# Kernel tuning notes

Hardware: AMD Instinct MI355X
Metric: run time of the kernel (lower is better)

Reference implementation:

```python
import jax, jax.numpy as jnp
import numpy as np

T, B = 256, 64
VOCAB, EMBED, HIDDEN, LAYERS, TAGS = 50000, 512, 512, 2, 9
H = HIDDEN // 2  # per-direction hidden size


def setup_inputs() -> dict:
    key = jax.random.key(0)
    ks = jax.random.split(key, 11)
    s = 0.05
    embed_table = jax.random.normal(ks[1], (VOCAB, EMBED), dtype=jnp.float32) * s
    embed_table = embed_table.at[0].set(0.0)  # padding_idx=0 row is zero
    return {
        "x": jax.random.randint(ks[0], (T, B), 1, VOCAB),  # ids >=1 -> full lengths
        "embed_table": embed_table,
        "w_ih": jax.random.normal(ks[2], (LAYERS, 2, 4 * H, HIDDEN), dtype=jnp.float32) * s,
        "w_hh": jax.random.normal(ks[3], (LAYERS, 2, 4 * H, H), dtype=jnp.float32) * s,
        "b_ih": jax.random.normal(ks[4], (LAYERS, 2, 4 * H), dtype=jnp.float32) * s,
        "b_hh": jax.random.normal(ks[5], (LAYERS, 2, 4 * H), dtype=jnp.float32) * s,
        "out_w": jax.random.normal(ks[6], (TAGS, HIDDEN), dtype=jnp.float32) * s,
        "out_b": jax.random.normal(ks[7], (TAGS,), dtype=jnp.float32) * s,
        "start_trans": jax.random.normal(ks[8], (TAGS,), dtype=jnp.float32) * s,
        "end_trans": jax.random.normal(ks[9], (TAGS,), dtype=jnp.float32) * s,
        "trans": jax.random.normal(ks[10], (TAGS, TAGS), dtype=jnp.float32) * s,
    }


def _lstm_dir(xs, Wih, Whh, b, reverse):
    """One LSTM direction over time-major xs [T,B,D]; PyTorch gate order i,f,g,o."""
    bsz = xs.shape[1]
    h0 = jnp.zeros((bsz, H), xs.dtype)
    c0 = jnp.zeros((bsz, H), xs.dtype)

    def step(carry, xt):
        h, c = carry
        g = xt @ Wih.T + h @ Whh.T + b
        i, f, gg, o = jnp.split(g, 4, axis=-1)
        c = jax.nn.sigmoid(f) * c + jax.nn.sigmoid(i) * jnp.tanh(gg)
        h = jax.nn.sigmoid(o) * jnp.tanh(c)
        return (h, c), h

    _, hs = jax.lax.scan(step, (h0, c0), xs, reverse=reverse)
    return hs  # [T,B,H], aligned to input time order


def _emissions(x, embed_table, w_ih, w_hh, b_ih, b_hh, out_w, out_b):
    seq = embed_table[x]  # [T,B,EMBED]
    for l in range(LAYERS):
        fwd = _lstm_dir(seq, w_ih[l, 0], w_hh[l, 0], b_ih[l, 0] + b_hh[l, 0], False)
        bwd = _lstm_dir(seq, w_ih[l, 1], w_hh[l, 1], b_ih[l, 1] + b_hh[l, 1], True)
        seq = jnp.concatenate([fwd, bwd], axis=-1)  # [T,B,HIDDEN]
    return seq @ out_w.T + out_b  # [T,B,TAGS]


def reference(x, embed_table, w_ih, w_hh, b_ih, b_hh, out_w, out_b,
              start_trans, end_trans, trans):
    em = _emissions(x, embed_table, w_ih, w_hh, b_ih, b_hh, out_w, out_b)

    # Viterbi decode (all sequences full-length since ids >= 1)
    score0 = start_trans[None, :] + em[0]  # [B,TAGS]

    def vstep(score, em_t):
        tot = score[:, :, None] + trans[None, :, :]  # [B,prev,cur]
        best_prev = jnp.argmax(tot, axis=1)          # [B,cur]
        return jnp.max(tot, axis=1) + em_t, best_prev

    score, history = jax.lax.scan(vstep, score0, em[1:])  # history: [T-1,B,TAGS]
    score = score + end_trans[None, :]
    best_last = jnp.argmax(score, axis=-1)   # [B]
    best_score = jnp.max(score, axis=-1)     # [B]

    def btstep(tag, idx_t):
        prev = jnp.take_along_axis(idx_t, tag[:, None], axis=1)[:, 0]
        return prev, prev

    _, prevs = jax.lax.scan(btstep, best_last, history, reverse=True)  # [T-1,B]
    tags = jnp.concatenate([prevs, best_last[None, :]], axis=0)        # [T,B]
    return tags.T, best_score  # ([B,T] best paths, [B] path scores)
```

## Files before the change

### kernel.cpp

```cpp
#include <hip/hip_runtime.h>
#include <math.h>

#define TAGS 9

static __device__ __forceinline__ float sigmoidf_(float x) {
  return 1.0f / (1.0f + expf(-x));
}

__global__ void k_transpose_whh(const float* __restrict__ whh, float* __restrict__ whhT) {
  __shared__ float tile[64][65];
  int bid = blockIdx.x;
  int ld = bid >> 6;
  int rt = (bid >> 2) & 15;
  int kt = bid & 3;
  const float* in = whh + (size_t)ld * 1024 * 256;
  float* out = whhT + (size_t)ld * 256 * 1024;
  int tid = threadIdx.x;
  int lr = tid >> 6;
  int lc = tid & 63;
#pragma unroll
  for (int i = 0; i < 16; i++) {
    int r = rt * 64 + i * 4 + lr;
    tile[lc][i * 4 + lr] = in[(size_t)r * 256 + kt * 64 + lc];
  }
  __syncthreads();
#pragma unroll
  for (int i = 0; i < 16; i++) {
    int k = kt * 64 + i * 4 + lr;
    out[(size_t)k * 1024 + rt * 64 + lc] = tile[i * 4 + lr][lc];
  }
}

__global__ void k_gather(const int* __restrict__ x, const float* __restrict__ table,
                         float* __restrict__ seq) {
  int tid = blockIdx.x * 256 + threadIdx.x;
  int row = tid >> 7;
  int e4 = tid & 127;
  int idx = x[row];
  const float4* src = (const float4*)(table + (size_t)idx * 512);
  float4* dst = (float4*)(seq + (size_t)row * 512);
  dst[e4] = src[e4];
}

__global__ __launch_bounds__(256, 2)
void k_gemm_nt(const float* __restrict__ A, const float* __restrict__ W,
               const float* __restrict__ bias1, const float* __restrict__ bias2,
               float* __restrict__ C, int M, int N, int K) {
  __shared__ float As[16][132];
  __shared__ float Ws[16][132];
  int tid = threadIdx.x;
  int tx = tid & 15, ty = tid >> 4;
  int n0 = blockIdx.x * 128, m0 = blockIdx.y * 128;
  int lr = tid >> 2;
  int lk = (tid & 3) * 4;
  float acc[8][8];
#pragma unroll
  for (int i = 0; i < 8; i++)
#pragma unroll
    for (int j = 0; j < 8; j++) acc[i][j] = 0.f;
  const float* Ab = A + (size_t)m0 * K;
  const float* Wb = W + (size_t)n0 * K;
  for (int k0 = 0; k0 < K; k0 += 16) {
    float4 a0 = *(const float4*)&Ab[(size_t)lr * K + k0 + lk];
    float4 a1 = *(const float4*)&Ab[(size_t)(lr + 64) * K + k0 + lk];
    float4 w0 = *(const float4*)&Wb[(size_t)lr * K + k0 + lk];
    float4 w1 = *(const float4*)&Wb[(size_t)(lr + 64) * K + k0 + lk];
    __syncthreads();
    As[lk + 0][lr] = a0.x; As[lk + 1][lr] = a0.y; As[lk + 2][lr] = a0.z; As[lk + 3][lr] = a0.w;
    As[lk + 0][lr + 64] = a1.x; As[lk + 1][lr + 64] = a1.y; As[lk + 2][lr + 64] = a1.z; As[lk + 3][lr + 64] = a1.w;
    Ws[lk + 0][lr] = w0.x; Ws[lk + 1][lr] = w0.y; Ws[lk + 2][lr] = w0.z; Ws[lk + 3][lr] = w0.w;
    Ws[lk + 0][lr + 64] = w1.x; Ws[lk + 1][lr + 64] = w1.y; Ws[lk + 2][lr + 64] = w1.z; Ws[lk + 3][lr + 64] = w1.w;
    __syncthreads();
#pragma unroll
    for (int kk = 0; kk < 16; kk++) {
      float4 av0 = *(const float4*)&As[kk][ty * 4];
      float4 av1 = *(const float4*)&As[kk][ty * 4 + 64];
      float4 wv0 = *(const float4*)&Ws[kk][tx * 4];
      float4 wv1 = *(const float4*)&Ws[kk][tx * 4 + 64];
      float am[8] = {av0.x, av0.y, av0.z, av0.w, av1.x, av1.y, av1.z, av1.w};
      float wn[8] = {wv0.x, wv0.y, wv0.z, wv0.w, wv1.x, wv1.y, wv1.z, wv1.w};
#pragma unroll
      for (int i = 0; i < 8; i++)
#pragma unroll
        for (int j = 0; j < 8; j++) acc[i][j] += am[i] * wn[j];
    }
  }
  float bsum[8];
#pragma unroll
  for (int j = 0; j < 8; j++) {
    int n = n0 + ((j < 4) ? (tx * 4 + j) : (64 + tx * 4 + (j - 4)));
    bsum[j] = bias1[n] + bias2[n];
  }
#pragma unroll
  for (int i = 0; i < 8; i++) {
    int m = m0 + ((i < 4) ? (ty * 4 + i) : (64 + ty * 4 + (i - 4)));
    float4 o0 = {acc[i][0] + bsum[0], acc[i][1] + bsum[1], acc[i][2] + bsum[2], acc[i][3] + bsum[3]};
    float4 o1 = {acc[i][4] + bsum[4], acc[i][5] + bsum[5], acc[i][6] + bsum[6], acc[i][7] + bsum[7]};
    *(float4*)&C[(size_t)m * N + n0 + tx * 4] = o0;
    *(float4*)&C[(size_t)m * N + n0 + 64 + tx * 4] = o1;
  }
}

#define FMA4(ACC, WV, S) { ACC.x += WV.x * (S); ACC.y += WV.y * (S); ACC.z += WV.z * (S); ACC.w += WV.w * (S); }
__global__ __launch_bounds__(512, 1)
void k_lstm(const float* __restrict__ gates_in,
            const float* __restrict__ whhT2,
            float* __restrict__ seq_out) {
  int wg = blockIdx.x;
  int dir = wg & 1;
  int b0 = (wg >> 1) * 2;
  const float* wT = whhT2 + (size_t)dir * 256 * 1024;
  int tid = threadIdx.x;
  int kh = tid >> 8;
  int j4 = (tid & 255) * 4;
  int bs = kh, u = tid & 255;
  __shared__ float h_lds[2][256];
  __shared__ float part[2][2][1024];
  h_lds[kh][u] = 0.f;
  float c = 0.f;
  __syncthreads();
  const int khbase = kh * 128;
  const float* wbase = wT + (size_t)khbase * 1024 + j4;
  for (int tt = 0; tt < 256; tt++) {
    int t = dir ? (255 - tt) : tt;
    float4 acc0, acc1;
    if (kh == 0) {
      const float* gi = gates_in + (size_t)(t * 64 + b0) * 2048 + dir * 1024 + j4;
      acc0 = *(const float4*)gi;
      acc1 = *(const float4*)(gi + 2048);
    } else {
      acc0 = float4{0.f, 0.f, 0.f, 0.f};
      acc1 = float4{0.f, 0.f, 0.f, 0.f};
    }
#pragma unroll 4
    for (int k = 0; k < 128; k += 4) {
      float4 ha = *(const float4*)&h_lds[0][khbase + k];
      float4 hb = *(const float4*)&h_lds[1][khbase + k];
      const float* w = wbase + (size_t)k * 1024;
      float4 w0 = *(const float4*)(w);
      float4 w1 = *(const float4*)(w + 1024);
      float4 w2 = *(const float4*)(w + 2048);
      float4 w3 = *(const float4*)(w + 3072);
      FMA4(acc0, w0, ha.x) FMA4(acc0, w1, ha.y) FMA4(acc0, w2, ha.z) FMA4(acc0, w3, ha.w)
      FMA4(acc1, w0, hb.x) FMA4(acc1, w1, hb.y) FMA4(acc1, w2, hb.z) FMA4(acc1, w3, hb.w)
    }
    *(float4*)&part[kh][0][j4] = acc0;
    *(float4*)&part[kh][1][j4] = acc1;
    __syncthreads();
    float gi_ = part[0][bs][u]       + part[1][bs][u];
    float gf  = part[0][bs][256 + u] + part[1][bs][256 + u];
    float gg  = part[0][bs][512 + u] + part[1][bs][512 + u];
    float go  = part[0][bs][768 + u] + part[1][bs][768 + u];
    c = sigmoidf_(gf) * c + sigmoidf_(gi_) * tanhf(gg);
    float h = sigmoidf_(go) * tanhf(c);
    h_lds[bs][u] = h;
    seq_out[(size_t)(t * 64 + b0 + bs) * 512 + dir * 256 + u] = h;
    __syncthreads();
  }
}

__global__ void k_emis(const float* __restrict__ seq, const float* __restrict__ out_w,
                       const float* __restrict__ out_b, float* __restrict__ em) {
  __shared__ float ow[TAGS * 512];
  int tid = threadIdx.x;
  for (int i = tid; i < TAGS * 512; i += 256) ow[i] = out_w[i];
  __syncthreads();
  int lane = tid & 63;
  int row = blockIdx.x * 4 + (tid >> 6);
  const float* s = seq + (size_t)row * 512;
  float p[TAGS];
#pragma unroll
  for (int t = 0; t < TAGS; t++) p[t] = 0.f;
#pragma unroll
  for (int kk = 0; kk < 8; kk++) {
    float sv = s[lane + kk * 64];
#pragma unroll
    for (int t = 0; t < TAGS; t++) p[t] += sv * ow[t * 512 + lane + kk * 64];
  }
#pragma unroll
  for (int t = 0; t < TAGS; t++) {
    float v = p[t];
#pragma unroll
    for (int off = 32; off > 0; off >>= 1) v += __shfl_down(v, off, 64);
    if (lane == 0) em[(size_t)row * TAGS + t] = v + out_b[t];
  }
}

__global__ void k_viterbi(const float* __restrict__ em, const float* __restrict__ start_t,
                          const float* __restrict__ end_t, const float* __restrict__ trans,
                          float* __restrict__ out) {
  int b = blockIdx.x;
  int lane = threadIdx.x;
  __shared__ unsigned char hist[255 * TAGS];
  float tin[TAGS];
#pragma unroll
  for (int p = 0; p < TAGS; p++) tin[p] = (lane < TAGS) ? trans[p * TAGS + lane] : 0.f;
  float score = -1e30f;
  if (lane < TAGS) score = start_t[lane] + em[(size_t)b * TAGS + lane];
  for (int t = 1; t < 256; t++) {
    float best = -1e30f; int bp = 0;
#pragma unroll
    for (int p = 0; p < TAGS; p++) {
      float v = __shfl(score, p, 64) + tin[p];
      if (v > best) { best = v; bp = p; }
    }
    if (lane < TAGS) {
      score = best + em[(size_t)(t * 64 + b) * TAGS + lane];
      hist[(t - 1) * TAGS + lane] = (unsigned char)bp;
    }
  }
  float fin = (lane < TAGS) ? (score + end_t[lane]) : -1e30f;
  float bsc = -1e30f; int bl = 0;
#pragma unroll
  for (int p = 0; p < TAGS; p++) {
    float v = __shfl(fin, p, 64);
    if (v > bsc) { bsc = v; bl = p; }
  }
  __syncthreads();
  if (lane == 0) {
    out[(size_t)16384 + b] = bsc;
    int tag = bl;
    out[(size_t)b * 256 + 255] = (float)tag;
    for (int t = 254; t >= 0; t--) {
      tag = hist[t * TAGS + tag];
      out[(size_t)b * 256 + t] = (float)tag;
    }
  }
}

extern "C" void kernel_launch(void* const* d_in, const int* in_sizes, int n_in,
                              void* d_out, int out_size, void* d_ws, size_t ws_size,
                              hipStream_t stream) {
  const int*   x       = (const int*)d_in[0];
  const float* table   = (const float*)d_in[1];
  const float* w_ih    = (const float*)d_in[2];
  const float* w_hh    = (const float*)d_in[3];
  const float* b_ih    = (const float*)d_in[4];
  const float* b_hh    = (const float*)d_in[5];
  const float* out_w   = (const float*)d_in[6];
  const float* out_b   = (const float*)d_in[7];
  const float* start_t = (const float*)d_in[8];
  const float* end_t   = (const float*)d_in[9];
  const float* trans   = (const float*)d_in[10];
  float* out = (float*)d_out;
  float* ws = (float*)d_ws;

  float* whhT  = ws;
  float* seq0  = whhT + 1048576;
  float* seq1  = seq0 + 8388608;
  float* gates = seq1 + 8388608;
  float* em    = gates + 33554432;

  k_transpose_whh<<<256, 256, 0, stream>>>(w_hh, whhT);
  k_gather<<<8192, 256, 0, stream>>>(x, table, seq0);

  dim3 gg(16, 128);
  k_gemm_nt<<<gg, 256, 0, stream>>>(seq0, w_ih, b_ih, b_hh, gates, 16384, 2048, 512);
  k_lstm<<<64, 512, 0, stream>>>(gates, whhT, seq1);
  k_gemm_nt<<<gg, 256, 0, stream>>>(seq1, w_ih + 1048576, b_ih + 2048, b_hh + 2048, gates, 16384, 2048, 512);
  k_lstm<<<64, 512, 0, stream>>>(gates, whhT + 524288, seq0);
  k_emis<<<4096, 256, 0, stream>>>(seq0, out_w, out_b, em);
  k_viterbi<<<64, 64, 0, stream>>>(em, start_t, end_t, trans, out);
}
```

Baseline: 5.347 ms.

## Split LSTM recurrence across 256 workgroups with grid-wide barrier per timestep

The LSTM recurrence moves from 64 workgroups (each owning two batch rows and reading the full recurrent weight matrix from global memory every step) to 256 workgroups, each owning two hidden units for all 64 batch rows. Each workgroup keeps its small weight slice in LDS, exchanges h through a double-buffered global buffer, and synchronises every timestep with an atomic-counter grid barrier. The input-projection GEMM is transposed so it writes gates in a time/unit/batch layout matched to the new recurrence, and the separate weight-transpose kernel is dropped. This spreads the serial recurrence over more compute units and removes the repeated weight streaming. In exchange it adds 255 grid-wide barriers per layer, global round-trips of h, and relies on all 256 workgroups being co-resident.

```diff
diff --git a/kernel.cpp b/kernel.cpp
--- a/kernel.cpp
+++ b/kernel.cpp
@@ -2,33 +2,10 @@
 #include <math.h>
 
 #define TAGS 9
+#define NWG 256
 
 static __device__ __forceinline__ float sigmoidf_(float x) {
   return 1.0f / (1.0f + expf(-x));
-}
-
-__global__ void k_transpose_whh(const float* __restrict__ whh, float* __restrict__ whhT) {
-  __shared__ float tile[64][65];
-  int bid = blockIdx.x;
-  int ld = bid >> 6;
-  int rt = (bid >> 2) & 15;
-  int kt = bid & 3;
-  const float* in = whh + (size_t)ld * 1024 * 256;
-  float* out = whhT + (size_t)ld * 256 * 1024;
-  int tid = threadIdx.x;
-  int lr = tid >> 6;
-  int lc = tid & 63;
-#pragma unroll
-  for (int i = 0; i < 16; i++) {
-    int r = rt * 64 + i * 4 + lr;
-    tile[lc][i * 4 + lr] = in[(size_t)r * 256 + kt * 64 + lc];
-  }
-  __syncthreads();
-#pragma unroll
-  for (int i = 0; i < 16; i++) {
-    int k = kt * 64 + i * 4 + lr;
-    out[(size_t)k * 1024 + rt * 64 + lc] = tile[i * 4 + lr][lc];
-  }
 }
 
 __global__ void k_gather(const int* __restrict__ x, const float* __restrict__ table,
@@ -43,11 +20,11 @@
 }
 
 __global__ __launch_bounds__(256, 2)
-void k_gemm_nt(const float* __restrict__ A, const float* __restrict__ W,
-               const float* __restrict__ bias1, const float* __restrict__ bias2,
-               float* __restrict__ C, int M, int N, int K) {
+void k_gemm_gates(const float* __restrict__ A, const float* __restrict__ B,
+                  const float* __restrict__ bias1, const float* __restrict__ bias2,
+                  float* __restrict__ gatesT) {
   __shared__ float As[16][132];
-  __shared__ float Ws[16][132];
+  __shared__ float Bs[16][132];
   int tid = threadIdx.x;
   int tx = tid & 15, ty = tid >> 4;
   int n0 = blockIdx.x * 128, m0 = blockIdx.y * 128;
@@ -58,104 +35,151 @@
   for (int i = 0; i < 8; i++)
 #pragma unroll
     for (int j = 0; j < 8; j++) acc[i][j] = 0.f;
-  const float* Ab = A + (size_t)m0 * K;
-  const float* Wb = W + (size_t)n0 * K;
-  for (int k0 = 0; k0 < K; k0 += 16) {
-    float4 a0 = *(const float4*)&Ab[(size_t)lr * K + k0 + lk];
-    float4 a1 = *(const float4*)&Ab[(size_t)(lr + 64) * K + k0 + lk];
-    float4 w0 = *(const float4*)&Wb[(size_t)lr * K + k0 + lk];
-    float4 w1 = *(const float4*)&Wb[(size_t)(lr + 64) * K + k0 + lk];
+  const float* Ab = A + (size_t)m0 * 512;
+  const float* Bb = B + (size_t)n0 * 512;
+  for (int k0 = 0; k0 < 512; k0 += 16) {
+    float4 a0 = *(const float4*)&Ab[(size_t)lr * 512 + k0 + lk];
+    float4 a1 = *(const float4*)&Ab[(size_t)(lr + 64) * 512 + k0 + lk];
+    float4 w0 = *(const float4*)&Bb[(size_t)lr * 512 + k0 + lk];
+    float4 w1 = *(const float4*)&Bb[(size_t)(lr + 64) * 512 + k0 + lk];
     __syncthreads();
     As[lk + 0][lr] = a0.x; As[lk + 1][lr] = a0.y; As[lk + 2][lr] = a0.z; As[lk + 3][lr] = a0.w;
     As[lk + 0][lr + 64] = a1.x; As[lk + 1][lr + 64] = a1.y; As[lk + 2][lr + 64] = a1.z; As[lk + 3][lr + 64] = a1.w;
-    Ws[lk + 0][lr] = w0.x; Ws[lk + 1][lr] = w0.y; Ws[lk + 2][lr] = w0.z; Ws[lk + 3][lr] = w0.w;
-    Ws[lk + 0][lr + 64] = w1.x; Ws[lk + 1][lr + 64] = w1.y; Ws[lk + 2][lr + 64] = w1.z; Ws[lk + 3][lr + 64] = w1.w;
+    Bs[lk + 0][lr] = w0.x; Bs[lk + 1][lr] = w0.y; Bs[lk + 2][lr] = w0.z; Bs[lk + 3][lr] = w0.w;
+    Bs[lk + 0][lr + 64] = w1.x; Bs[lk + 1][lr + 64] = w1.y; Bs[lk + 2][lr + 64] = w1.z; Bs[lk + 3][lr + 64] = w1.w;
     __syncthreads();
 #pragma unroll
     for (int kk = 0; kk < 16; kk++) {
       float4 av0 = *(const float4*)&As[kk][ty * 4];
       float4 av1 = *(const float4*)&As[kk][ty * 4 + 64];
-      float4 wv0 = *(const float4*)&Ws[kk][tx * 4];
-      float4 wv1 = *(const float4*)&Ws[kk][tx * 4 + 64];
+      float4 bv0 = *(const float4*)&Bs[kk][tx * 4];
+      float4 bv1 = *(const float4*)&Bs[kk][tx * 4 + 64];
       float am[8] = {av0.x, av0.y, av0.z, av0.w, av1.x, av1.y, av1.z, av1.w};
-      float wn[8] = {wv0.x, wv0.y, wv0.z, wv0.w, wv1.x, wv1.y, wv1.z, wv1.w};
+      float bn[8] = {bv0.x, bv0.y, bv0.z, bv0.w, bv1.x, bv1.y, bv1.z, bv1.w};
 #pragma unroll
       for (int i = 0; i < 8; i++)
 #pragma unroll
-        for (int j = 0; j < 8; j++) acc[i][j] += am[i] * wn[j];
-    }
-  }
-  float bsum[8];
-#pragma unroll
-  for (int j = 0; j < 8; j++) {
-    int n = n0 + ((j < 4) ? (tx * 4 + j) : (64 + tx * 4 + (j - 4)));
-    bsum[j] = bias1[n] + bias2[n];
-  }
+        for (int j = 0; j < 8; j++) acc[i][j] += am[i] * bn[j];
+    }
+  }
+  int t0 = n0 >> 6;
 #pragma unroll
   for (int i = 0; i < 8; i++) {
     int m = m0 + ((i < 4) ? (ty * 4 + i) : (64 + ty * 4 + (i - 4)));
-    float4 o0 = {acc[i][0] + bsum[0], acc[i][1] + bsum[1], acc[i][2] + bsum[2], acc[i][3] + bsum[3]};
-    float4 o1 = {acc[i][4] + bsum[4], acc[i][5] + bsum[5], acc[i][6] + bsum[6], acc[i][7] + bsum[7]};
-    *(float4*)&C[(size_t)m * N + n0 + tx * 4] = o0;
-    *(float4*)&C[(size_t)m * N + n0 + 64 + tx * 4] = o1;
-  }
-}
-
-#define FMA4(ACC, WV, S) { ACC.x += WV.x * (S); ACC.y += WV.y * (S); ACC.z += WV.z * (S); ACC.w += WV.w * (S); }
-__global__ __launch_bounds__(512, 1)
-void k_lstm(const float* __restrict__ gates_in,
-            const float* __restrict__ whhT2,
-            float* __restrict__ seq_out) {
-  int wg = blockIdx.x;
-  int dir = wg & 1;
-  int b0 = (wg >> 1) * 2;
-  const float* wT = whhT2 + (size_t)dir * 256 * 1024;
-  int tid = threadIdx.x;
-  int kh = tid >> 8;
-  int j4 = (tid & 255) * 4;
-  int bs = kh, u = tid & 255;
-  __shared__ float h_lds[2][256];
-  __shared__ float part[2][2][1024];
-  h_lds[kh][u] = 0.f;
+    float bs = bias1[m] + bias2[m];
+    float4 o0 = {acc[i][0] + bs, acc[i][1] + bs, acc[i][2] + bs, acc[i][3] + bs};
+    float4 o1 = {acc[i][4] + bs, acc[i][5] + bs, acc[i][6] + bs, acc[i][7] + bs};
+    *(float4*)&gatesT[((size_t)t0 * 2048 + m) * 64 + tx * 4] = o0;
+    *(float4*)&gatesT[((size_t)(t0 + 1) * 2048 + m) * 64 + tx * 4] = o1;
+  }
+}
+
+__global__ __launch_bounds__(512)
+void k_lstm_rec(const float* __restrict__ gatesT,
+                const float* __restrict__ whh,
+                float* __restrict__ seq_out,
+                float* __restrict__ hbuf,
+                int* __restrict__ gbar,
+                int gen_base) {
+  __shared__ float h_s[256 * 64];
+  __shared__ float w_s[8][256];
+  __shared__ float g_p[64 * 64];
+  int wg = blockIdx.x, tid = threadIdx.x;
+  int d = wg & 1, ug = wg >> 1;
+  int b = tid & 63, ks = tid >> 6;
+  {
+    int gate = ks >> 1, uo = ks & 1;
+    const float* src = whh + ((size_t)d * 1024 + gate * 256 + ug * 2 + uo) * 256;
+    *(float4*)&w_s[ks][b * 4] = *(const float4*)&src[b * 4];
+  }
+  if (tid < 128) hbuf[(size_t)wg * 128 + tid] = 0.f;
+  int mygen = gen_base;
   float c = 0.f;
-  __syncthreads();
-  const int khbase = kh * 128;
-  const float* wbase = wT + (size_t)khbase * 1024 + j4;
+
+  auto BAR = [&]() {
+    __syncthreads();
+    if (tid == 0) {
+      mygen++;
+      int prev = __hip_atomic_fetch_add(&gbar[0], 1, __ATOMIC_RELEASE, __HIP_MEMORY_SCOPE_AGENT);
+      if (prev == NWG - 1) {
+        __hip_atomic_store(&gbar[0], 0, __ATOMIC_RELAXED, __HIP_MEMORY_SCOPE_AGENT);
+        __hip_atomic_store(&gbar[1], mygen, __ATOMIC_RELEASE, __HIP_MEMORY_SCOPE_AGENT);
+      } else {
+        while (__hip_atomic_load(&gbar[1], __ATOMIC_RELAXED, __HIP_MEMORY_SCOPE_AGENT) < mygen)
+          __builtin_amdgcn_s_sleep(2);
+      }
+      __builtin_amdgcn_fence(__ATOMIC_ACQUIRE, "agent");
+    }
+    __syncthreads();
+  };
+
+  BAR();
+
   for (int tt = 0; tt < 256; tt++) {
-    int t = dir ? (255 - tt) : tt;
-    float4 acc0, acc1;
-    if (kh == 0) {
-      const float* gi = gates_in + (size_t)(t * 64 + b0) * 2048 + dir * 1024 + j4;
-      acc0 = *(const float4*)gi;
-      acc1 = *(const float4*)(gi + 2048);
-    } else {
-      acc0 = float4{0.f, 0.f, 0.f, 0.f};
-      acc1 = float4{0.f, 0.f, 0.f, 0.f};
-    }
-#pragma unroll 4
-    for (int k = 0; k < 128; k += 4) {
-      float4 ha = *(const float4*)&h_lds[0][khbase + k];
-      float4 hb = *(const float4*)&h_lds[1][khbase + k];
-      const float* w = wbase + (size_t)k * 1024;
-      float4 w0 = *(const float4*)(w);
-      float4 w1 = *(const float4*)(w + 1024);
-      float4 w2 = *(const float4*)(w + 2048);
-      float4 w3 = *(const float4*)(w + 3072);
-      FMA4(acc0, w0, ha.x) FMA4(acc0, w1, ha.y) FMA4(acc0, w2, ha.z) FMA4(acc0, w3, ha.w)
-      FMA4(acc1, w0, hb.x) FMA4(acc1, w1, hb.y) FMA4(acc1, w2, hb.z) FMA4(acc1, w3, hb.w)
-    }
-    *(float4*)&part[kh][0][j4] = acc0;
-    *(float4*)&part[kh][1][j4] = acc1;
-    __syncthreads();
-    float gi_ = part[0][bs][u]       + part[1][bs][u];
-    float gf  = part[0][bs][256 + u] + part[1][bs][256 + u];
-    float gg  = part[0][bs][512 + u] + part[1][bs][512 + u];
-    float go  = part[0][bs][768 + u] + part[1][bs][768 + u];
-    c = sigmoidf_(gf) * c + sigmoidf_(gi_) * tanhf(gg);
-    float h = sigmoidf_(go) * tanhf(c);
-    h_lds[bs][u] = h;
-    seq_out[(size_t)(t * 64 + b0 + bs) * 512 + dir * 256 + u] = h;
-    __syncthreads();
+    int t = d ? (255 - tt) : tt;
+    float gin0 = 0.f, gin1 = 0.f, gin2 = 0.f, gin3 = 0.f;
+    if (ks < 2) {
+      int u = ug * 2 + ks;
+      const float* gp = gatesT + ((size_t)t * 2048 + d * 1024 + u) * 64 + b;
+      gin0 = gp[0];
+      gin1 = gp[(size_t)256 * 64];
+      gin2 = gp[(size_t)512 * 64];
+      gin3 = gp[(size_t)768 * 64];
+    }
+    {
+      const float* hsrc = hbuf + (size_t)(tt & 1) * 32768 + (size_t)d * 16384;
+#pragma unroll
+      for (int i = 0; i < 8; i++) {
+        int f = tid + i * 512;
+        int bb = f >> 6;
+        int k4 = (f & 63) * 4;
+        float4 v = *(const float4*)&hsrc[(size_t)f * 4];
+        int col = bb ^ ((k4 >> 2) & 63);
+        h_s[(k4 + 0) * 64 + col] = v.x;
+        h_s[(k4 + 1) * 64 + col] = v.y;
+        h_s[(k4 + 2) * 64 + col] = v.z;
+        h_s[(k4 + 3) * 64 + col] = v.w;
+      }
+    }
+    __syncthreads();
+    float pr[8];
+#pragma unroll
+    for (int r = 0; r < 8; r++) pr[r] = 0.f;
+    int kb = ks * 32;
+#pragma unroll
+    for (int kk = 0; kk < 32; kk += 4) {
+      int k = kb + kk;
+      int col = b ^ ((k >> 2) & 63);
+      float h0 = h_s[(k + 0) * 64 + col];
+      float h1 = h_s[(k + 1) * 64 + col];
+      float h2 = h_s[(k + 2) * 64 + col];
+      float h3 = h_s[(k + 3) * 64 + col];
+#pragma unroll
+      for (int r = 0; r < 8; r++) {
+        float4 wv = *(const float4*)&w_s[r][k];
+        pr[r] += wv.x * h0 + wv.y * h1 + wv.z * h2 + wv.w * h3;
+      }
+    }
+#pragma unroll
+    for (int r = 0; r < 8; r++) g_p[(ks * 8 + r) * 64 + b] = pr[r];
+    __syncthreads();
+    if (ks < 2) {
+      int u = ug * 2 + ks;
+      float gv[4] = {gin0, gin1, gin2, gin3};
+#pragma unroll
+      for (int g = 0; g < 4; g++) {
+        int row = g * 2 + ks;
+        float s = gv[g];
+#pragma unroll
+        for (int q = 0; q < 8; q++) s += g_p[(q * 8 + row) * 64 + b];
+        gv[g] = s;
+      }
+      c = sigmoidf_(gv[1]) * c + sigmoidf_(gv[0]) * tanhf(gv[2]);
+      float h = sigmoidf_(gv[3]) * tanhf(c);
+      hbuf[(size_t)((tt + 1) & 1) * 32768 + (size_t)d * 16384 + (size_t)b * 256 + u] = h;
+      seq_out[((size_t)t * 64 + b) * 512 + d * 256 + u] = h;
+    }
+    if (tt < 255) BAR();
   }
 }
 
@@ -245,20 +269,21 @@
   float* out = (float*)d_out;
   float* ws = (float*)d_ws;
 
-  float* whhT  = ws;
-  float* seq0  = whhT + 1048576;
-  float* seq1  = seq0 + 8388608;
-  float* gates = seq1 + 8388608;
-  float* em    = gates + 33554432;
-
-  k_transpose_whh<<<256, 256, 0, stream>>>(w_hh, whhT);
+  float* seq0   = ws;
+  float* seq1   = seq0 + 8388608;
+  float* gatesT = seq1 + 8388608;
+  float* em     = gatesT + 33554432;
+  float* hbuf   = em + 147456;
+  int*   barp   = (int*)(hbuf + 65536);
+
+  hipMemsetAsync(barp, 0, 2 * sizeof(int), stream);
   k_gather<<<8192, 256, 0, stream>>>(x, table, seq0);
 
-  dim3 gg(16, 128);
-  k_gemm_nt<<<gg, 256, 0, stream>>>(seq0, w_ih, b_ih, b_hh, gates, 16384, 2048, 512);
-  k_lstm<<<64, 512, 0, stream>>>(gates, whhT, seq1);
-  k_gemm_nt<<<gg, 256, 0, stream>>>(seq1, w_ih + 1048576, b_ih + 2048, b_hh + 2048, gates, 16384, 2048, 512);
-  k_lstm<<<64, 512, 0, stream>>>(gates, whhT + 524288, seq0);
+  dim3 gg(128, 16);
+  k_gemm_gates<<<gg, 256, 0, stream>>>(w_ih, seq0, b_ih, b_hh, gatesT);
+  k_lstm_rec<<<NWG, 512, 0, stream>>>(gatesT, w_hh, seq1, hbuf, barp, 0);
+  k_gemm_gates<<<gg, 256, 0, stream>>>(w_ih + 1048576, seq1, b_ih + 2048, b_hh + 2048, gatesT);
+  k_lstm_rec<<<NWG, 512, 0, stream>>>(gatesT, w_hh + 524288, seq0, hbuf, barp, 256);
   k_emis<<<4096, 256, 0, stream>>>(seq0, out_w, out_b, em);
   k_viterbi<<<64, 64, 0, stream>>>(em, start_t, end_t, trans, out);
 }
```

Result: slower. 12.27 ms (+129.5%).
